# Performance work log

Hardware: AMD Instinct MI355X
Metric: run time of the kernel (lower is better)

Reference implementation:

```python
import jax, jax.numpy as jnp
import numpy as np

N_NODES = 100000
N_EDGES = 1600000
C_IN = 128
C_OUT = 128
BN_EPS = 1e-5


def setup_inputs() -> dict:
    key = jax.random.key(0)
    k = jax.random.split(key, 4)
    x = jax.random.normal(k[0], (N_NODES, C_IN), dtype=jnp.float32)
    edge_index = jax.random.randint(k[1], (2, N_EDGES), 0, N_NODES, dtype=jnp.int32)
    # nn.Linear params (Kaiming-uniform-ish scale)
    lim = 1.0 / np.sqrt(C_IN)
    W = jax.random.uniform(k[2], (C_IN, C_OUT), jnp.float32, -lim, lim)
    b = jnp.zeros((C_OUT,), jnp.float32)
    # BatchNorm (eval mode: running stats)
    gamma = jnp.ones((C_OUT,), jnp.float32)
    beta = jnp.zeros((C_OUT,), jnp.float32)
    running_mean = jnp.zeros((C_OUT,), jnp.float32)
    running_var = jnp.ones((C_OUT,), jnp.float32)
    return {"x": x, "edge_index": edge_index, "W": W, "b": b,
            "gamma": gamma, "beta": beta,
            "running_mean": running_mean, "running_var": running_var}


def reference(x, edge_index, W, b, gamma, beta, running_mean, running_var):
    # Linear projection: [N, C_in] @ [C_in, C_out]
    h = x @ W + b
    in_node, out_node = edge_index[0], edge_index[1]
    # gather edge features then scatter-mean onto destination nodes
    sums = jax.ops.segment_sum(h[in_node], out_node, num_segments=N_NODES)
    cnt = jax.ops.segment_sum(jnp.ones((in_node.shape[0],), h.dtype), out_node,
                              num_segments=N_NODES)
    agg = sums / jnp.maximum(cnt, 1.0)[:, None]  # mean; 0 for isolated nodes
    # BatchNorm1d (eval mode: running stats) + ReLU; dropout is identity in eval
    inv = jax.lax.rsqrt(running_var + BN_EPS)
    out = (agg - running_mean) * (inv * gamma) + beta
    return jax.nn.relu(out)
```

## Files before the change

kernel.cpp:

```cpp
#include <hip/hip_runtime.h>


#define NN 100000
#define NE 1600000
#define CC 128
#define BN_EPS 1e-5f
#define LBLK 1563
#define LSTR 136
#define NBUK 256
#define DPB 391
#define ACH 4096
#define ABLK 391
#define BCAP 7168
#define CAP 12288
#define GNB 64
#define CAP2 4096
#define BHS 16

typedef __attribute__((ext_vector_type(8))) short bf16x8;
typedef __attribute__((ext_vector_type(4))) float f32x4;

static __device__ __forceinline__ short f2bf(float f) {
  union { float f; unsigned u; } v; v.f = f;
  unsigned r = (v.u + 0x7FFF + ((v.u >> 16) & 1)) >> 16;
  return (short)r;
}
static __device__ __forceinline__ float bflo(unsigned p) {
  return __uint_as_float(p << 16);
}
static __device__ __forceinline__ float bfhi(unsigned p) {
  return __uint_as_float(p & 0xffff0000u);
}

static __device__ __forceinline__ int excl_scan256(int* a, int t, int v) {
  a[t] = v;
  __syncthreads();
  for (int d = 1; d < 256; d <<= 1) {
    const int x = (t >= d) ? a[t - d] : 0;
    __syncthreads();
    a[t] += x;
    __syncthreads();
  }
  const int incl = a[t];
  __syncthreads();
  a[t] = incl - v;
  __syncthreads();
  return incl - v;
}

__global__ __launch_bounds__(256) void scatter_linear2(
    const int* __restrict__ ei, int* __restrict__ gcur,
    int* __restrict__ ebuf, const float* __restrict__ x,
    const float* __restrict__ W, const float* __restrict__ bias,
    short* __restrict__ hout, int scat) {
  __shared__ __align__(16) char smem[50176];
  const int t = threadIdx.x;

  if (blockIdx.x < scat) {
    int2* sorted = (int2*)smem;
    int*  lh     = (int*)(smem + 32768);
    int*  lex    = (int*)(smem + 33792);
    int*  rb     = (int*)(smem + 34816);
    int*  lc     = (int*)(smem + 35840);
    const int e0 = blockIdx.x * ACH;
    const int e1 = min(NE, e0 + ACH);
    lh[t] = 0;
    __syncthreads();
    for (int e = e0 + t; e < e1; e += 256) atomicAdd(&lh[ei[NE + e] / DPB], 1);
    __syncthreads();
    const int vh = lh[t];
    const int lbase = excl_scan256(lex, t, vh);
    lc[t] = lbase;
    if (vh > 0) rb[t] = t * BCAP + atomicAdd(&gcur[t * BHS], vh);
    __syncthreads();
    for (int e = e0 + t; e < e1; e += 256) {
      const int src = ei[e], dst = ei[NE + e];
      const int p = atomicAdd(&lc[dst / DPB], 1);
      sorted[p] = make_int2(src, dst);
    }
    __syncthreads();
    const int n = e1 - e0;
    for (int i = t; i < n; i += 256) {
      const int2 v = sorted[i];
      const int b = v.y / DPB;
      ebuf[rb[b] + (i - lex[b])] = (v.x << 9) | (v.y - b * DPB);
    }
    return;
  }

  short* lsA = (short*)smem;
  short* lsW = (short*)(smem + 17408);
  const int n0 = (blockIdx.x - scat) * 64;

#pragma unroll
  for (int j = 0; j < 8; ++j) {
    const int idx = j * 256 + t;
    const int row = idx >> 5, kc4 = idx & 31;
    float4 v = make_float4(0.f, 0.f, 0.f, 0.f);
    if (n0 + row < NN) v = *(const float4*)(x + (size_t)(n0 + row) * CC + kc4 * 4);
    short4 sv;
    sv.x = f2bf(v.x); sv.y = f2bf(v.y); sv.z = f2bf(v.z); sv.w = f2bf(v.w);
    *(short4*)(lsA + row * LSTR + kc4 * 4) = sv;
  }
  for (int j = 0; j < 64; ++j) {
    const int i = j * 256 + t;
    const int k = i >> 7, n = i & 127;
    const int nt = n & 7, m2 = n >> 3;
    const int kb = k >> 5, q = (k >> 3) & 3, jj = k & 7;
    lsW[((nt * 4 + kb) * 64 + (m2 + 16 * q)) * 8 + jj] = f2bf(W[i]);
  }
  __syncthreads();

  const int wave = t >> 6, lane = t & 63;
  const int quad = lane >> 4, m = lane & 15;
  const int rowbase = n0 + wave * 16;

  f32x4 acc[8];
#pragma unroll
  for (int nt = 0; nt < 8; ++nt) acc[nt] = (f32x4){0.f, 0.f, 0.f, 0.f};

#pragma unroll
  for (int kb = 0; kb < 4; ++kb) {
    const bf16x8 a =
        *(const bf16x8*)(lsA + (wave * 16 + m) * LSTR + kb * 32 + quad * 8);
#pragma unroll
    for (int nt = 0; nt < 8; ++nt) {
      const bf16x8 bb = *(const bf16x8*)(lsW + (size_t)(((nt * 4 + kb) * 64 + lane) * 8));
      acc[nt] = __builtin_amdgcn_mfma_f32_16x16x32_bf16(a, bb, acc[nt], 0, 0, 0);
    }
  }

  const float4 b0 = *(const float4*)(bias + m * 8);
  const float4 b1 = *(const float4*)(bias + m * 8 + 4);
  const float bv[8] = {b0.x, b0.y, b0.z, b0.w, b1.x, b1.y, b1.z, b1.w};

#pragma unroll
  for (int reg = 0; reg < 4; ++reg) {
    const int R = rowbase + quad * 4 + reg;
    if (R >= NN) continue;
    bf16x8 hv;
#pragma unroll
    for (int nt = 0; nt < 8; ++nt) hv[nt] = f2bf(acc[nt][reg] + bv[nt]);
    *(bf16x8*)(hout + (size_t)R * CC + m * 8) = hv;
  }
}

__global__ __launch_bounds__(1024) void bucket_to_csr2(
    const int* __restrict__ ebuf, const int* __restrict__ gcur,
    int* __restrict__ off, int* __restrict__ dg, int* __restrict__ csr) {
  __shared__ int dh[512];
  __shared__ int s[512];
  __shared__ int lcur[512];
  __shared__ int lcsr[CAP];
  const int b = blockIdx.x, t = threadIdx.x;

  const int seglen = min(gcur[b * BHS], BCAP);
  const int segbase = b * BCAP;
  const int lo = b * DPB;
  const int hi = min(NN, lo + DPB);
  const int nd = hi - lo;
  const int* eb = ebuf + segbase;

  if (t < 512) dh[t] = 0;
  __syncthreads();
  for (int i = t; i < seglen; i += 1024) atomicAdd(&dh[eb[i] & 511], 1);
  __syncthreads();

  if (t < 512) s[t] = dh[t];
  __syncthreads();
  for (int d = 1; d < 512; d <<= 1) {
    int a0 = 0;
    if (t < 512 && t >= d) a0 = s[t - d];
    __syncthreads();
    if (t < 512) s[t] += a0;
    __syncthreads();
  }
  if (t < 512) lcur[t] = s[t] - dh[t];
  if (t < nd) {
    off[lo + t] = segbase + (s[t] - dh[t]);
    dg[lo + t] = dh[t];
  }
  if (b == NBUK - 1 && t == 0) off[NN] = segbase + seglen;
  __syncthreads();

  if (seglen <= CAP) {
    for (int i = t; i < seglen; i += 1024) {
      const int e = eb[i];
      const int p = atomicAdd(&lcur[e & 511], 1);
      lcsr[p] = (int)((unsigned)e >> 9);
    }
    __syncthreads();
    for (int i = t; i < seglen; i += 1024) csr[segbase + i] = lcsr[i];
  } else {
    for (int i = t; i < seglen; i += 1024) {
      const int e = eb[i];
      const int p = atomicAdd(&lcur[e & 511], 1);
      csr[segbase + p] = (int)((unsigned)e >> 9);
    }
  }
}

__global__ __launch_bounds__(256) void gather_bn_relu2(
    const short* __restrict__ h, const int* __restrict__ off,
    const int* __restrict__ dg, const int* __restrict__ csr,
    const float* __restrict__ gamma, const float* __restrict__ beta,
    const float* __restrict__ rmean, const float* __restrict__ rvar,
    float* __restrict__ out) {
  __shared__ int loff[GNB + 1];
  __shared__ int ldg[GNB];
  __shared__ int lcsr[CAP2];
  const int nb0 = blockIdx.x * GNB;
  const int t = threadIdx.x;
  const int nnb = min(GNB, NN - nb0);

  for (int i = t; i <= nnb; i += 256) loff[i] = off[nb0 + i];
  if (t < nnb) ldg[t] = dg[nb0 + t];
  __syncthreads();
  const int s0 = loff[0];
  const int seglen = loff[nnb] - s0;
  const int stg = min(seglen, CAP2);
  for (int i = t; i < stg; i += 256) lcsr[i] = csr[s0 + i];
  __syncthreads();

  const int wave = t >> 6, lane = t & 63;
  const int e4 = lane >> 4;
  const int c16 = lane & 15;
  const float4 g0 = *(const float4*)(gamma + c16 * 8);
  const float4 g1 = *(const float4*)(gamma + c16 * 8 + 4);
  const float4 v0 = *(const float4*)(rvar + c16 * 8);
  const float4 v1 = *(const float4*)(rvar + c16 * 8 + 4);
  const float4 m0 = *(const float4*)(rmean + c16 * 8);
  const float4 m1 = *(const float4*)(rmean + c16 * 8 + 4);
  const float4 bt0 = *(const float4*)(beta + c16 * 8);
  const float4 bt1 = *(const float4*)(beta + c16 * 8 + 4);
  float4 sc0, sc1, sh0, sh1;
  sc0.x = g0.x * rsqrtf(v0.x + BN_EPS); sh0.x = bt0.x - m0.x * sc0.x;
  sc0.y = g0.y * rsqrtf(v0.y + BN_EPS); sh0.y = bt0.y - m0.y * sc0.y;
  sc0.z = g0.z * rsqrtf(v0.z + BN_EPS); sh0.z = bt0.z - m0.z * sc0.z;
  sc0.w = g0.w * rsqrtf(v0.w + BN_EPS); sh0.w = bt0.w - m0.w * sc0.w;
  sc1.x = g1.x * rsqrtf(v1.x + BN_EPS); sh1.x = bt1.x - m1.x * sc1.x;
  sc1.y = g1.y * rsqrtf(v1.y + BN_EPS); sh1.y = bt1.y - m1.y * sc1.y;
  sc1.z = g1.z * rsqrtf(v1.z + BN_EPS); sh1.z = bt1.z - m1.z * sc1.z;
  sc1.w = g1.w * rsqrtf(v1.w + BN_EPS); sh1.w = bt1.w - m1.w * sc1.w;

  const int lEnd = min(nnb, wave * 16 + 16);
  const bool inl = (seglen <= CAP2);
  for (int l = wave * 16; l < lEnd; ++l) {
    const int deg = ldg[l];
    const int s = inl ? loff[l] - s0 : loff[l];
    const int e = s + deg;
    float a0 = 0.f, a1 = 0.f, a2 = 0.f, a3 = 0.f;
    float a4 = 0.f, a5 = 0.f, a6 = 0.f, a7 = 0.f;
    int i = s + e4;
    for (; i + 4 < e; i += 8) {
      const int q0 = inl ? lcsr[i] : csr[i];
      const int q1 = inl ? lcsr[i + 4] : csr[i + 4];
      const uint4 p0 = *(const uint4*)(h + (size_t)q0 * CC + c16 * 8);
      const uint4 p1 = *(const uint4*)(h + (size_t)q1 * CC + c16 * 8);
      a0 += bflo(p0.x) + bflo(p1.x); a1 += bfhi(p0.x) + bfhi(p1.x);
      a2 += bflo(p0.y) + bflo(p1.y); a3 += bfhi(p0.y) + bfhi(p1.y);
      a4 += bflo(p0.z) + bflo(p1.z); a5 += bfhi(p0.z) + bfhi(p1.z);
      a6 += bflo(p0.w) + bflo(p1.w); a7 += bfhi(p0.w) + bfhi(p1.w);
    }
    if (i < e) {
      const int q = inl ? lcsr[i] : csr[i];
      const uint4 p = *(const uint4*)(h + (size_t)q * CC + c16 * 8);
      a0 += bflo(p.x); a1 += bfhi(p.x);
      a2 += bflo(p.y); a3 += bfhi(p.y);
      a4 += bflo(p.z); a5 += bfhi(p.z);
      a6 += bflo(p.w); a7 += bfhi(p.w);
    }
    a0 += __shfl_xor(a0, 16); a1 += __shfl_xor(a1, 16);
    a2 += __shfl_xor(a2, 16); a3 += __shfl_xor(a3, 16);
    a4 += __shfl_xor(a4, 16); a5 += __shfl_xor(a5, 16);
    a6 += __shfl_xor(a6, 16); a7 += __shfl_xor(a7, 16);
    a0 += __shfl_xor(a0, 32); a1 += __shfl_xor(a1, 32);
    a2 += __shfl_xor(a2, 32); a3 += __shfl_xor(a3, 32);
    a4 += __shfl_xor(a4, 32); a5 += __shfl_xor(a5, 32);
    a6 += __shfl_xor(a6, 32); a7 += __shfl_xor(a7, 32);
    if (e4 == 0) {
      const float inv = (deg > 0) ? 1.0f / (float)deg : 0.0f;
      float4 o0, o1;
      o0.x = fmaxf(0.f, a0 * inv * sc0.x + sh0.x);
      o0.y = fmaxf(0.f, a1 * inv * sc0.y + sh0.y);
      o0.z = fmaxf(0.f, a2 * inv * sc0.z + sh0.z);
      o0.w = fmaxf(0.f, a3 * inv * sc0.w + sh0.w);
      o1.x = fmaxf(0.f, a4 * inv * sc1.x + sh1.x);
      o1.y = fmaxf(0.f, a5 * inv * sc1.y + sh1.y);
      o1.z = fmaxf(0.f, a6 * inv * sc1.z + sh1.z);
      o1.w = fmaxf(0.f, a7 * inv * sc1.w + sh1.w);
      float* op = out + (size_t)(nb0 + l) * CC + c16 * 8;
      *(float4*)op = o0;
      *(float4*)(op + 4) = o1;
    }
  }
}

__global__ __launch_bounds__(256) void edge_scatter(
    const float* __restrict__ x, const int* __restrict__ ei,
    float* __restrict__ sums, int* __restrict__ cnt) {
  int gt = blockIdx.x * 256 + threadIdx.x;
  int e = gt >> 5;
  int sub = gt & 31;
  if (e >= NE) return;
  int src = ei[e];
  int dst = ei[NE + e];
  const float4 v = *(const float4*)(x + (size_t)src * CC + sub * 4);
  float* o = sums + (size_t)dst * CC + sub * 4;
  unsafeAtomicAdd(o + 0, v.x);
  unsafeAtomicAdd(o + 1, v.y);
  unsafeAtomicAdd(o + 2, v.z);
  unsafeAtomicAdd(o + 3, v.w);
  if (sub == 0) atomicAdd(cnt + dst, 1);
}

__global__ __launch_bounds__(256) void gemm_bn_relu_fb(
    float* buf, const float* __restrict__ W, const float* __restrict__ bias,
    const float* __restrict__ gamma, const float* __restrict__ beta,
    const float* __restrict__ rmean, const float* __restrict__ rvar,
    const int* __restrict__ cnt) {
  __shared__ float xsT[CC][65];
  const int t = threadIdx.x;
  const int n0 = blockIdx.x * 64;
  for (int j = 0; j < 8; ++j) {
    int i = t + 256 * j;
    int row = i >> 5;
    int ko = (i & 31) * 4;
    float4 v = make_float4(0.f, 0.f, 0.f, 0.f);
    if (n0 + row < NN) v = *(const float4*)(buf + (size_t)(n0 + row) * CC + ko);
    xsT[ko + 0][row] = v.x;
    xsT[ko + 1][row] = v.y;
    xsT[ko + 2][row] = v.z;
    xsT[ko + 3][row] = v.w;
  }
  __syncthreads();
  const int cg = t & 31;
  const int ng8 = (t >> 5) * 8;
  float acc[8][4];
#pragma unroll
  for (int j = 0; j < 8; ++j)
#pragma unroll
    for (int c = 0; c < 4; ++c) acc[j][c] = 0.f;
#pragma unroll 8
  for (int k = 0; k < CC; ++k) {
    const float4 wv = *(const float4*)(W + k * CC + cg * 4);
#pragma unroll
    for (int j = 0; j < 8; ++j) {
      const float xv = xsT[k][ng8 + j];
      acc[j][0] = fmaf(xv, wv.x, acc[j][0]);
      acc[j][1] = fmaf(xv, wv.y, acc[j][1]);
      acc[j][2] = fmaf(xv, wv.z, acc[j][2]);
      acc[j][3] = fmaf(xv, wv.w, acc[j][3]);
    }
  }
  const float4 bb = *(const float4*)(bias + cg * 4);
  const float4 gg = *(const float4*)(gamma + cg * 4);
  const float4 bt = *(const float4*)(beta + cg * 4);
  const float4 mu = *(const float4*)(rmean + cg * 4);
  const float4 vr = *(const float4*)(rvar + cg * 4);
  float sc[4], sh[4];
  sc[0] = gg.x * rsqrtf(vr.x + BN_EPS);
  sc[1] = gg.y * rsqrtf(vr.y + BN_EPS);
  sc[2] = gg.z * rsqrtf(vr.z + BN_EPS);
  sc[3] = gg.w * rsqrtf(vr.w + BN_EPS);
  sh[0] = bt.x - mu.x * sc[0];
  sh[1] = bt.y - mu.y * sc[1];
  sh[2] = bt.z - mu.z * sc[2];
  sh[3] = bt.w - mu.w * sc[3];
#pragma unroll
  for (int j = 0; j < 8; ++j) {
    const int n = n0 + ng8 + j;
    if (n >= NN) continue;
    const int cn = cnt[n];
    const float inv = cn > 0 ? 1.0f / (float)cn : 0.0f;
    const float bsel = cn > 0 ? 1.0f : 0.0f;
    float4 o;
    o.x = fmaxf(0.f, (acc[j][0] * inv + bsel * bb.x) * sc[0] + sh[0]);
    o.y = fmaxf(0.f, (acc[j][1] * inv + bsel * bb.y) * sc[1] + sh[1]);
    o.z = fmaxf(0.f, (acc[j][2] * inv + bsel * bb.z) * sc[2] + sh[2]);
    o.w = fmaxf(0.f, (acc[j][3] * inv + bsel * bb.w) * sc[3] + sh[3]);
    *(float4*)(buf + (size_t)n * CC + cg * 4) = o;
  }
}

extern "C" void kernel_launch(void* const* d_in, const int* in_sizes, int n_in,
                              void* d_out, int out_size, void* d_ws, size_t ws_size,
                              hipStream_t stream) {
  const float* x     = (const float*)d_in[0];
  const int*   ei    = (const int*)d_in[1];
  const float* W     = (const float*)d_in[2];
  const float* bias  = (const float*)d_in[3];
  const float* gamma = (const float*)d_in[4];
  const float* beta  = (const float*)d_in[5];
  const float* rmean = (const float*)d_in[6];
  const float* rvar  = (const float*)d_in[7];
  float* out = (float*)d_out;

  const size_t OFF_B = 0;
  const size_t DG_B  = 400128;
  const size_t GC_B  = DG_B + 400128;
  const size_t EB_B  = GC_B + 16384;
  const size_t H_B   = EB_B + (size_t)NBUK * BCAP * 4;
  const size_t NEED  = H_B + (size_t)NN * CC * 2;

  const int GGRID = (NN + GNB - 1) / GNB;

  if (ws_size >= NEED) {
    int*   off  = (int*)((char*)d_ws + OFF_B);
    int*   dg   = (int*)((char*)d_ws + DG_B);
    int*   gcur = (int*)((char*)d_ws + GC_B);
    int*   ebuf = (int*)((char*)d_ws + EB_B);
    int*   csr  = ebuf;
    short* h    = (short*)((char*)d_ws + H_B);

    hipMemsetAsync(gcur, 0, 16384, stream);
    scatter_linear2<<<ABLK + LBLK, 256, 0, stream>>>(
        ei, gcur, ebuf, x, W, bias, h, ABLK);
    bucket_to_csr2<<<NBUK, 1024, 0, stream>>>(ebuf, gcur, off, dg, csr);
    gather_bn_relu2<<<GGRID, 256, 0, stream>>>(h, off, dg, csr, gamma, beta,
                                               rmean, rvar, out);
  } else {
    int* cnt = (int*)d_ws;
    hipMemsetAsync(out, 0, (size_t)NN * CC * sizeof(float), stream);
    hipMemsetAsync(cnt, 0, (size_t)NN * sizeof(int), stream);
    edge_scatter<<<(NE * 32) / 256, 256, 0, stream>>>(x, ei, out, cnt);
    gemm_bn_relu_fb<<<(NN + 63) / 64, 256, 0, stream>>>(
        out, W, bias, gamma, beta, rmean, rvar, cnt);
  }
}
```

Measured before the change: 218.1 us.

## Fuse bucket-to-CSR construction with neighbor gather and BN-ReLU into one kernel

Merges the CSR-building kernel and the gather/BatchNorm/ReLU kernel so each bucket block builds its local CSR in shared memory and immediately gathers features for its destination nodes. This removes the global off/dg/csr writes and reads and one kernel launch. In exchange the gather phase now runs on only 256 large blocks, reducing parallelism and latency hiding compared with the earlier finer-grained grid. It also drops the overflow path for buckets exceeding capacity, relying on BCAP clamping.

```diff
diff --git a/kernel.cpp b/kernel.cpp
--- a/kernel.cpp
+++ b/kernel.cpp
@@ -12,9 +12,6 @@
 #define ACH 4096
 #define ABLK 391
 #define BCAP 7168
-#define CAP 12288
-#define GNB 64
-#define CAP2 4096
 #define BHS 16
 
 typedef __attribute__((ext_vector_type(8))) short bf16x8;
@@ -145,27 +142,28 @@
   }
 }
 
-__global__ __launch_bounds__(1024) void bucket_to_csr2(
+__global__ __launch_bounds__(1024) void bucket_gather(
     const int* __restrict__ ebuf, const int* __restrict__ gcur,
-    int* __restrict__ off, int* __restrict__ dg, int* __restrict__ csr) {
+    const short* __restrict__ h, const float* __restrict__ gamma,
+    const float* __restrict__ beta, const float* __restrict__ rmean,
+    const float* __restrict__ rvar, float* __restrict__ out) {
+  __shared__ int leb[BCAP];
+  __shared__ int lcsr[BCAP];
   __shared__ int dh[512];
   __shared__ int s[512];
   __shared__ int lcur[512];
-  __shared__ int lcsr[CAP];
   const int b = blockIdx.x, t = threadIdx.x;
 
   const int seglen = min(gcur[b * BHS], BCAP);
-  const int segbase = b * BCAP;
   const int lo = b * DPB;
-  const int hi = min(NN, lo + DPB);
-  const int nd = hi - lo;
-  const int* eb = ebuf + segbase;
-
+  const int nd = min(NN - lo, DPB);
+  const int* eb = ebuf + (size_t)b * BCAP;
+
+  for (int i = t; i < seglen; i += 1024) leb[i] = eb[i];
   if (t < 512) dh[t] = 0;
   __syncthreads();
-  for (int i = t; i < seglen; i += 1024) atomicAdd(&dh[eb[i] & 511], 1);
-  __syncthreads();
-
+  for (int i = t; i < seglen; i += 1024) atomicAdd(&dh[leb[i] & 511], 1);
+  __syncthreads();
   if (t < 512) s[t] = dh[t];
   __syncthreads();
   for (int d = 1; d < 512; d <<= 1) {
@@ -176,50 +174,12 @@
     __syncthreads();
   }
   if (t < 512) lcur[t] = s[t] - dh[t];
-  if (t < nd) {
-    off[lo + t] = segbase + (s[t] - dh[t]);
-    dg[lo + t] = dh[t];
-  }
-  if (b == NBUK - 1 && t == 0) off[NN] = segbase + seglen;
-  __syncthreads();
-
-  if (seglen <= CAP) {
-    for (int i = t; i < seglen; i += 1024) {
-      const int e = eb[i];
-      const int p = atomicAdd(&lcur[e & 511], 1);
-      lcsr[p] = (int)((unsigned)e >> 9);
-    }
-    __syncthreads();
-    for (int i = t; i < seglen; i += 1024) csr[segbase + i] = lcsr[i];
-  } else {
-    for (int i = t; i < seglen; i += 1024) {
-      const int e = eb[i];
-      const int p = atomicAdd(&lcur[e & 511], 1);
-      csr[segbase + p] = (int)((unsigned)e >> 9);
-    }
-  }
-}
-
-__global__ __launch_bounds__(256) void gather_bn_relu2(
-    const short* __restrict__ h, const int* __restrict__ off,
-    const int* __restrict__ dg, const int* __restrict__ csr,
-    const float* __restrict__ gamma, const float* __restrict__ beta,
-    const float* __restrict__ rmean, const float* __restrict__ rvar,
-    float* __restrict__ out) {
-  __shared__ int loff[GNB + 1];
-  __shared__ int ldg[GNB];
-  __shared__ int lcsr[CAP2];
-  const int nb0 = blockIdx.x * GNB;
-  const int t = threadIdx.x;
-  const int nnb = min(GNB, NN - nb0);
-
-  for (int i = t; i <= nnb; i += 256) loff[i] = off[nb0 + i];
-  if (t < nnb) ldg[t] = dg[nb0 + t];
-  __syncthreads();
-  const int s0 = loff[0];
-  const int seglen = loff[nnb] - s0;
-  const int stg = min(seglen, CAP2);
-  for (int i = t; i < stg; i += 256) lcsr[i] = csr[s0 + i];
+  __syncthreads();
+  for (int i = t; i < seglen; i += 1024) {
+    const int e = leb[i];
+    const int p = atomicAdd(&lcur[e & 511], 1);
+    lcsr[p] = (int)((unsigned)e >> 9);
+  }
   __syncthreads();
 
   const int wave = t >> 6, lane = t & 63;
@@ -243,18 +203,15 @@
   sc1.z = g1.z * rsqrtf(v1.z + BN_EPS); sh1.z = bt1.z - m1.z * sc1.z;
   sc1.w = g1.w * rsqrtf(v1.w + BN_EPS); sh1.w = bt1.w - m1.w * sc1.w;
 
-  const int lEnd = min(nnb, wave * 16 + 16);
-  const bool inl = (seglen <= CAP2);
-  for (int l = wave * 16; l < lEnd; ++l) {
-    const int deg = ldg[l];
-    const int s = inl ? loff[l] - s0 : loff[l];
-    const int e = s + deg;
+  for (int l = wave; l < nd; l += 16) {
+    const int deg = dh[l];
+    const int sB = s[l] - deg;
+    const int e = sB + deg;
     float a0 = 0.f, a1 = 0.f, a2 = 0.f, a3 = 0.f;
     float a4 = 0.f, a5 = 0.f, a6 = 0.f, a7 = 0.f;
-    int i = s + e4;
+    int i = sB + e4;
     for (; i + 4 < e; i += 8) {
-      const int q0 = inl ? lcsr[i] : csr[i];
-      const int q1 = inl ? lcsr[i + 4] : csr[i + 4];
+      const int q0 = lcsr[i], q1 = lcsr[i + 4];
       const uint4 p0 = *(const uint4*)(h + (size_t)q0 * CC + c16 * 8);
       const uint4 p1 = *(const uint4*)(h + (size_t)q1 * CC + c16 * 8);
       a0 += bflo(p0.x) + bflo(p1.x); a1 += bfhi(p0.x) + bfhi(p1.x);
@@ -263,7 +220,7 @@
       a6 += bflo(p0.w) + bflo(p1.w); a7 += bfhi(p0.w) + bfhi(p1.w);
     }
     if (i < e) {
-      const int q = inl ? lcsr[i] : csr[i];
+      const int q = lcsr[i];
       const uint4 p = *(const uint4*)(h + (size_t)q * CC + c16 * 8);
       a0 += bflo(p.x); a1 += bfhi(p.x);
       a2 += bflo(p.y); a3 += bfhi(p.y);
@@ -289,7 +246,7 @@
       o1.y = fmaxf(0.f, a5 * inv * sc1.y + sh1.y);
       o1.z = fmaxf(0.f, a6 * inv * sc1.z + sh1.z);
       o1.w = fmaxf(0.f, a7 * inv * sc1.w + sh1.w);
-      float* op = out + (size_t)(nb0 + l) * CC + c16 * 8;
+      float* op = out + (size_t)(lo + l) * CC + c16 * 8;
       *(float4*)op = o0;
       *(float4*)(op + 4) = o1;
     }
@@ -396,29 +353,21 @@
   const float* rvar  = (const float*)d_in[7];
   float* out = (float*)d_out;
 
-  const size_t OFF_B = 0;
-  const size_t DG_B  = 400128;
-  const size_t GC_B  = DG_B + 400128;
-  const size_t EB_B  = GC_B + 16384;
-  const size_t H_B   = EB_B + (size_t)NBUK * BCAP * 4;
-  const size_t NEED  = H_B + (size_t)NN * CC * 2;
-
-  const int GGRID = (NN + GNB - 1) / GNB;
+  const size_t GC_B = 0;
+  const size_t EB_B = 16384;
+  const size_t H_B  = EB_B + (size_t)NBUK * BCAP * 4;
+  const size_t NEED = H_B + (size_t)NN * CC * 2;
 
   if (ws_size >= NEED) {
-    int*   off  = (int*)((char*)d_ws + OFF_B);
-    int*   dg   = (int*)((char*)d_ws + DG_B);
     int*   gcur = (int*)((char*)d_ws + GC_B);
     int*   ebuf = (int*)((char*)d_ws + EB_B);
-    int*   csr  = ebuf;
     short* h    = (short*)((char*)d_ws + H_B);
 
     hipMemsetAsync(gcur, 0, 16384, stream);
     scatter_linear2<<<ABLK + LBLK, 256, 0, stream>>>(
         ei, gcur, ebuf, x, W, bias, h, ABLK);
-    bucket_to_csr2<<<NBUK, 1024, 0, stream>>>(ebuf, gcur, off, dg, csr);
-    gather_bn_relu2<<<GGRID, 256, 0, stream>>>(h, off, dg, csr, gamma, beta,
-                                               rmean, rvar, out);
+    bucket_gather<<<NBUK, 1024, 0, stream>>>(ebuf, gcur, h, gamma, beta,
+                                             rmean, rvar, out);
   } else {
     int* cnt = (int*)d_ws;
     hipMemsetAsync(out, 0, (size_t)NN * CC * sizeof(float), stream);
```

Result: faster. 211.6 us (-3.0%).
